# Kernel tuning notes

Hardware: AMD Instinct MI355X
Metric: run time of the kernel (lower is better)

Reference implementation:

```python
import jax, jax.numpy as jnp
import numpy as np

SMOOTHNESS_RATIO = 0.2
DEGREE_RATIO = 0.1
SPARSITY_RATIO = 0.1
VERY_SMALL_NUMBER = 1e-12


def setup_inputs() -> dict:
    key = jax.random.key(0)
    k1, k2 = jax.random.split(key)
    B, N, D = 64, 1024, 16
    out_adj = jax.random.uniform(k1, (B, N, N), dtype=jnp.float32)  # nonneg adjacency (softmax-like)
    features = jax.random.normal(k2, (B, N, D), dtype=jnp.float32)
    return {"out_adj": out_adj, "features": features}


def reference(out_adj, features):
    # Faithful fused version of add_batch_graph_loss with keep_batch_dim=True.
    # Per sample i: smoothness_ratio * tr(F^T (diag(deg) - A) F) / (N*N)
    #   tr(F^T diag(deg) F) = sum_n deg_n ||f_n||^2
    #   tr(F^T A F)        = sum(F * (A @ F))
    B, N, _ = out_adj.shape
    denom = jnp.float32(N * N)

    deg = jnp.sum(out_adj, axis=-1)                       # [B, N] row degrees
    AF = jnp.einsum('bij,bjd->bid', out_adj, features)    # [B, N, D]
    smooth = (jnp.einsum('bn,bnd->b', deg, features * features)
              - jnp.einsum('bnd,bnd->b', features, AF))   # [B] = tr(F^T L F)
    graph_loss = SMOOTHNESS_RATIO * smooth / denom

    # degree regularization: -degree_ratio * ones^T log(A @ ones + eps) / N
    # A @ ones == deg
    log_degrees = jnp.log(deg + VERY_SMALL_NUMBER)        # [B, N]
    graph_loss = graph_loss - DEGREE_RATIO * jnp.sum(log_degrees, axis=-1) / N

    # sparsity: sparsity_ratio * sum(A^2) / (N*N)
    graph_loss = graph_loss + SPARSITY_RATIO * jnp.sum(out_adj * out_adj, axis=(1, 2)) / denom
    return graph_loss  # [B]
```

## Files before the change

### kernel.cpp

```cpp
#include <hip/hip_runtime.h>


#define NN      1024
#define DD      16
#define ROWS    64
#define TPB     256
#define SMOOTHR 0.2f
#define DEGRR   0.1f
#define SPARSR  0.1f
#define EPSV    1e-12f

__global__ __launch_bounds__(TPB)
void graph_loss_kernel(const float* __restrict__ A,
                       const float* __restrict__ F,
                       float* __restrict__ out) {
    __shared__ float fn_lds[ROWS][DD];
    __shared__ float fn2_lds[ROWS];
    __shared__ float degq[ROWS][65];
    __shared__ float wred[4][2];

    const int tid = threadIdx.x;
    const int bid = blockIdx.x;
    const int b   = bid >> 4;
    const int n0  = (bid & 15) * ROWS;

    const float* __restrict__ Fb = F + (size_t)b * NN * DD;
    const float* __restrict__ Ab = A + ((size_t)b * NN + n0) * NN;

    float4 fj[4][4];
    {
        const float* p = Fb + (size_t)(4 * tid) * DD;
        #pragma unroll
        for (int jj = 0; jj < 4; ++jj)
            #pragma unroll
            for (int q = 0; q < 4; ++q)
                fj[jj][q] = *(const float4*)(p + jj * DD + 4 * q);
    }

    {
        const int r = tid >> 2, q = tid & 3;
        *(float4*)&fn_lds[r][4 * q] =
            *(const float4*)(Fb + (size_t)(n0 + r) * DD + 4 * q);
    }
    __syncthreads();
    if (tid < ROWS) {
        float s = 0.f;
        #pragma unroll
        for (int d = 0; d < DD; ++d) s += fn_lds[tid][d] * fn_lds[tid][d];
        fn2_lds[tid] = s;
    }
    __syncthreads();

    float sm = 0.f, sq = 0.f;

    const float* __restrict__ arow = Ab + 4 * tid;
    const int  g       = tid >> 2;
    const bool deglane = (tid & 3) == 0;

    auto process = [&](const float4 a, const int r) {
        float s = (a.x + a.y) + (a.z + a.w);
        s += __shfl_xor(s, 1);
        s += __shfl_xor(s, 2);
        if (deglane) degq[r][g] = s;

        sq += a.x * a.x + a.y * a.y + a.z * a.z + a.w * a.w;

        float dt0 = 0.f, dt1 = 0.f, dt2 = 0.f, dt3 = 0.f;
        #pragma unroll
        for (int q = 0; q < 4; ++q) {
            const float4 f = *(const float4*)&fn_lds[r][4 * q];
            dt0 += fj[0][q].x * f.x + fj[0][q].y * f.y + fj[0][q].z * f.z + fj[0][q].w * f.w;
            dt1 += fj[1][q].x * f.x + fj[1][q].y * f.y + fj[1][q].z * f.z + fj[1][q].w * f.w;
            dt2 += fj[2][q].x * f.x + fj[2][q].y * f.y + fj[2][q].z * f.z + fj[2][q].w * f.w;
            dt3 += fj[3][q].x * f.x + fj[3][q].y * f.y + fj[3][q].z * f.z + fj[3][q].w * f.w;
        }
        const float fn2 = fn2_lds[r];
        sm += a.x * (fn2 - dt0) + a.y * (fn2 - dt1)
            + a.z * (fn2 - dt2) + a.w * (fn2 - dt3);
    };

    #define LOADR(r) (*(const float4*)(arow + (size_t)(r) * NN))
    float4 a0 = LOADR(0), a1 = LOADR(1), a2 = LOADR(2), a3 = LOADR(3);

    #pragma unroll 1
    for (int rb = 0; rb < ROWS - 4; rb += 4) {
        const float4 t0 = a0, t1 = a1, t2 = a2, t3 = a3;
        a0 = LOADR(rb + 4);
        a1 = LOADR(rb + 5);
        a2 = LOADR(rb + 6);
        a3 = LOADR(rb + 7);
        process(t0, rb + 0);
        process(t1, rb + 1);
        process(t2, rb + 2);
        process(t3, rb + 3);
    }
    process(a0, ROWS - 4);
    process(a1, ROWS - 3);
    process(a2, ROWS - 2);
    process(a3, ROWS - 1);
    #undef LOADR

    __syncthreads();
    float lg = 0.f;
    if (tid < ROWS) {
        float s = 0.f;
        #pragma unroll 1
        for (int i = 0; i < ROWS; ++i) s += degq[tid][i];
        lg = logf(s + EPSV);
    }

    #pragma unroll
    for (int m = 1; m < 64; m <<= 1) {
        sm += __shfl_xor(sm, m);
        sq += __shfl_xor(sq, m);
        lg += __shfl_xor(lg, m);
    }
    const int w = tid >> 6;
    if ((tid & 63) == 0) { wred[w][0] = sm; wred[w][1] = sq; }
    __syncthreads();
    if (tid == 0) {
        float S = 0.f, Q = 0.f;
        #pragma unroll
        for (int i = 0; i < 4; ++i) { S += wred[i][0]; Q += wred[i][1]; }
        const float denom = (float)NN * (float)NN;
        const float contrib = SMOOTHR * S / denom
                            - DEGRR * lg / (float)NN
                            + SPARSR * Q / denom;
        atomicAdd(out + b, contrib);
    }
}

extern "C" void kernel_launch(void* const* d_in, const int* in_sizes, int n_in,
                              void* d_out, int out_size, void* d_ws, size_t ws_size,
                              hipStream_t stream) {
    const float* A = (const float*)d_in[0];
    const float* F = (const float*)d_in[1];
    float* out = (float*)d_out;

    const int B = out_size;
    hipMemsetAsync(d_out, 0, (size_t)B * sizeof(float), stream);
    graph_loss_kernel<<<dim3(B * (NN / ROWS)), dim3(TPB), 0, stream>>>(A, F, out);
}
```

Measured before the change: 371.8 us.

## Stream adjacency with nontemporal loads, read row features from global, shallower prefetch

```diff
diff --git a/kernel.cpp b/kernel.cpp
--- a/kernel.cpp
+++ b/kernel.cpp
@@ -10,11 +10,12 @@
 #define SPARSR  0.1f
 #define EPSV    1e-12f
 
+typedef float vf4 __attribute__((ext_vector_type(4)));
+
 __global__ __launch_bounds__(TPB)
 void graph_loss_kernel(const float* __restrict__ A,
                        const float* __restrict__ F,
                        float* __restrict__ out) {
-    __shared__ float fn_lds[ROWS][DD];
     __shared__ float fn2_lds[ROWS];
     __shared__ float degq[ROWS][65];
     __shared__ float wred[4][2];
@@ -27,26 +28,21 @@
     const float* __restrict__ Fb = F + (size_t)b * NN * DD;
     const float* __restrict__ Ab = A + ((size_t)b * NN + n0) * NN;
 
-    float4 fj[4][4];
+    vf4 fj[4][4];
     {
         const float* p = Fb + (size_t)(4 * tid) * DD;
         #pragma unroll
         for (int jj = 0; jj < 4; ++jj)
             #pragma unroll
             for (int q = 0; q < 4; ++q)
-                fj[jj][q] = *(const float4*)(p + jj * DD + 4 * q);
+                fj[jj][q] = *(const vf4*)(p + jj * DD + 4 * q);
     }
 
-    {
-        const int r = tid >> 2, q = tid & 3;
-        *(float4*)&fn_lds[r][4 * q] =
-            *(const float4*)(Fb + (size_t)(n0 + r) * DD + 4 * q);
-    }
-    __syncthreads();
     if (tid < ROWS) {
+        const float* p = Fb + (size_t)(n0 + tid) * DD;
         float s = 0.f;
         #pragma unroll
-        for (int d = 0; d < DD; ++d) s += fn_lds[tid][d] * fn_lds[tid][d];
+        for (int d = 0; d < DD; ++d) s += p[d] * p[d];
         fn2_lds[tid] = s;
     }
     __syncthreads();
@@ -57,7 +53,20 @@
     const int  g       = tid >> 2;
     const bool deglane = (tid & 3) == 0;
 
-    auto process = [&](const float4 a, const int r) {
+    #define LOADR(r) __builtin_nontemporal_load((const vf4*)(arow + (size_t)(r) * NN))
+    vf4 a0 = LOADR(0);
+    vf4 a1 = LOADR(1);
+
+    #pragma unroll 1
+    for (int r = 0; r < ROWS; ++r) {
+        const vf4 a = a0;
+        a0 = a1;
+        if (r + 2 < ROWS) a1 = LOADR(r + 2);
+
+        const vf4* __restrict__ Fr = (const vf4*)(Fb + (size_t)(n0 + r) * DD);
+        const vf4 f0 = Fr[0], f1 = Fr[1], f2 = Fr[2], f3 = Fr[3];
+        const float fn2 = fn2_lds[r];
+
         float s = (a.x + a.y) + (a.z + a.w);
         s += __shfl_xor(s, 1);
         s += __shfl_xor(s, 2);
@@ -65,39 +74,27 @@
 
         sq += a.x * a.x + a.y * a.y + a.z * a.z + a.w * a.w;
 
-        float dt0 = 0.f, dt1 = 0.f, dt2 = 0.f, dt3 = 0.f;
-        #pragma unroll
-        for (int q = 0; q < 4; ++q) {
-            const float4 f = *(const float4*)&fn_lds[r][4 * q];
-            dt0 += fj[0][q].x * f.x + fj[0][q].y * f.y + fj[0][q].z * f.z + fj[0][q].w * f.w;
-            dt1 += fj[1][q].x * f.x + fj[1][q].y * f.y + fj[1][q].z * f.z + fj[1][q].w * f.w;
-            dt2 += fj[2][q].x * f.x + fj[2][q].y * f.y + fj[2][q].z * f.z + fj[2][q].w * f.w;
-            dt3 += fj[3][q].x * f.x + fj[3][q].y * f.y + fj[3][q].z * f.z + fj[3][q].w * f.w;
-        }
-        const float fn2 = fn2_lds[r];
+        float dt0, dt1, dt2, dt3;
+        dt0  = fj[0][0].x * f0.x + fj[0][0].y * f0.y + fj[0][0].z * f0.z + fj[0][0].w * f0.w;
+        dt0 += fj[0][1].x * f1.x + fj[0][1].y * f1.y + fj[0][1].z * f1.z + fj[0][1].w * f1.w;
+        dt0 += fj[0][2].x * f2.x + fj[0][2].y * f2.y + fj[0][2].z * f2.z + fj[0][2].w * f2.w;
+        dt0 += fj[0][3].x * f3.x + fj[0][3].y * f3.y + fj[0][3].z * f3.z + fj[0][3].w * f3.w;
+        dt1  = fj[1][0].x * f0.x + fj[1][0].y * f0.y + fj[1][0].z * f0.z + fj[1][0].w * f0.w;
+        dt1 += fj[1][1].x * f1.x + fj[1][1].y * f1.y + fj[1][1].z * f1.z + fj[1][1].w * f1.w;
+        dt1 += fj[1][2].x * f2.x + fj[1][2].y * f2.y + fj[1][2].z * f2.z + fj[1][2].w * f2.w;
+        dt1 += fj[1][3].x * f3.x + fj[1][3].y * f3.y + fj[1][3].z * f3.z + fj[1][3].w * f3.w;
+        dt2  = fj[2][0].x * f0.x + fj[2][0].y * f0.y + fj[2][0].z * f0.z + fj[2][0].w * f0.w;
+        dt2 += fj[2][1].x * f1.x + fj[2][1].y * f1.y + fj[2][1].z * f1.z + fj[2][1].w * f1.w;
+        dt2 += fj[2][2].x * f2.x + fj[2][2].y * f2.y + fj[2][2].z * f2.z + fj[2][2].w * f2.w;
+        dt2 += fj[2][3].x * f3.x + fj[2][3].y * f3.y + fj[2][3].z * f3.z + fj[2][3].w * f3.w;
+        dt3  = fj[3][0].x * f0.x + fj[3][0].y * f0.y + fj[3][0].z * f0.z + fj[3][0].w * f0.w;
+        dt3 += fj[3][1].x * f1.x + fj[3][1].y * f1.y + fj[3][1].z * f1.z + fj[3][1].w * f1.w;
+        dt3 += fj[3][2].x * f2.x + fj[3][2].y * f2.y + fj[3][2].z * f2.z + fj[3][2].w * f2.w;
+        dt3 += fj[3][3].x * f3.x + fj[3][3].y * f3.y + fj[3][3].z * f3.z + fj[3][3].w * f3.w;
+
         sm += a.x * (fn2 - dt0) + a.y * (fn2 - dt1)
             + a.z * (fn2 - dt2) + a.w * (fn2 - dt3);
-    };
-
-    #define LOADR(r) (*(const float4*)(arow + (size_t)(r) * NN))
-    float4 a0 = LOADR(0), a1 = LOADR(1), a2 = LOADR(2), a3 = LOADR(3);
-
-    #pragma unroll 1
-    for (int rb = 0; rb < ROWS - 4; rb += 4) {
-        const float4 t0 = a0, t1 = a1, t2 = a2, t3 = a3;
-        a0 = LOADR(rb + 4);
-        a1 = LOADR(rb + 5);
-        a2 = LOADR(rb + 6);
-        a3 = LOADR(rb + 7);
-        process(t0, rb + 0);
-        process(t1, rb + 1);
-        process(t2, rb + 2);
-        process(t3, rb + 3);
     }
-    process(a0, ROWS - 4);
-    process(a1, ROWS - 3);
-    process(a2, ROWS - 2);
-    process(a3, ROWS - 1);
     #undef LOADR
 
     __syncthreads();
@@ -138,6 +135,6 @@
     float* out = (float*)d_out;
 
     const int B = out_size;
-    hipMemsetAsync(d_out, 0, (size_t)B * sizeof(float), stream);
+    (void)hipMemsetAsync(d_out, 0, (size_t)B * sizeof(float), stream);
     graph_loss_kernel<<<dim3(B * (NN / ROWS)), dim3(TPB), 0, stream>>>(A, F, out);
 }
```

Result: no change. 366.5 us (-1.4%).
